# Performance work log

Hardware: AMD Instinct MI355X
Metric: run time of the kernel (lower is better)

The kernel has to match this reference:

```python
import jax, jax.numpy as jnp
import numpy as np

B, T, C = 8, 1024, 768
H, D = 12, 64

def setup_inputs() -> dict:
    key = jax.random.key(0)
    ks = jax.random.split(key, 6)
    s = 0.02
    return {
        "x": jax.random.normal(ks[0], (B, T, C), dtype=jnp.float32),
        "Wq": jax.random.normal(ks[1], (H, C, D), dtype=jnp.float32) * s,
        "Wk": jax.random.normal(ks[2], (H, C, D), dtype=jnp.float32) * s,
        "Wv": jax.random.normal(ks[3], (H, C, D), dtype=jnp.float32) * s,
        "Wproj": jax.random.normal(ks[4], (C, C), dtype=jnp.float32) * s,
        "bproj": jnp.zeros((C,), dtype=jnp.float32),
    }

def reference(x, Wq, Wk, Wv, Wproj, bproj):
    # per-head projections, vectorized over heads: [B,H,T,D]
    q = jnp.einsum('btc,hcd->bhtd', x, Wq)
    k = jnp.einsum('btc,hcd->bhtd', x, Wk)
    v = jnp.einsum('btc,hcd->bhtd', x, Wv)
    scale = 1.0 / jnp.sqrt(jnp.asarray(q.shape[-1], q.dtype))
    scores = jnp.einsum('bhtd,bhsd->bhts', q, k) * scale  # [B,H,T,T]
    attn = jax.nn.softmax(scores, axis=-1)
    out = jnp.einsum('bhts,bhsd->bhtd', attn, v)          # [B,H,T,D]
    # concat heads along last dim -> [B,T,H*D]
    out = out.transpose(0, 2, 1, 3).reshape(x.shape[0], x.shape[1], -1)
    return out @ Wproj + bproj
```

## Files before the change

### kernel.cpp

```cpp
#include <hip/hip_runtime.h>
#include <hip/hip_bf16.h>

using u16 = unsigned short;

typedef __attribute__((ext_vector_type(8))) short bf16x8;
typedef __attribute__((ext_vector_type(4))) float f32x4;
typedef __attribute__((ext_vector_type(16))) float f32x16;

#define B_ 8
#define T_ 1024
#define C_ 768
#define H_ 12
#define D_ 64

typedef const void __attribute__((address_space(1))) gv_t;
typedef void __attribute__((address_space(3))) lv_t;

__device__ __forceinline__ void gload_lds16(const void* g, void* l) {
  __builtin_amdgcn_global_load_lds((gv_t*)g, (lv_t*)l, 16, 0, 0);
}

__device__ __forceinline__ u16 f2b(float f) {
  union { float f; unsigned u; } a; a.f = f;
  unsigned r = a.u + 0x7FFFu + ((a.u >> 16) & 1u);
  return (u16)(r >> 16);
}

__device__ __forceinline__ float fexp2(float x) {
  float r;
  asm("v_exp_f32 %0, %1" : "=v"(r) : "v"(x));
  return r;
}

__device__ __forceinline__ unsigned cvtpk_bf16(float lo, float hi) {
  unsigned r;
  asm("v_cvt_pk_bf16_f32 %0, %1, %2" : "=v"(r) : "v"(lo), "v"(hi));
  return r;
}
__device__ __forceinline__ void plane32_swap(unsigned &a, unsigned &b) {
  asm volatile("v_permlane32_swap_b32 %0, %1" : "+v"(a), "+v"(b));
}

__global__ __launch_bounds__(256) void prep_all(
    const float* __restrict__ x,
    const float* __restrict__ Wq, const float* __restrict__ Wk,
    const float* __restrict__ Wv, const float* __restrict__ Wp,
    u16* __restrict__ Xb, u16* __restrict__ Wqkvt, u16* __restrict__ Wpt)
{
  int bb = blockIdx.x;
  if (bb < 3072) {
    int i = (bb * 256 + threadIdx.x) * 8;
    float4 a = *(const float4*)(x + i);
    float4 b = *(const float4*)(x + i + 4);
    union { bf16x8 v; u16 s[8]; } o;
    o.s[0] = f2b(a.x); o.s[1] = f2b(a.y); o.s[2] = f2b(a.z); o.s[3] = f2b(a.w);
    o.s[4] = f2b(b.x); o.s[5] = f2b(b.y); o.s[6] = f2b(b.z); o.s[7] = f2b(b.w);
    *(bf16x8*)(Xb + i) = o.v;
  } else {
    int idx = (bb - 3072) * 256 + threadIdx.x;
    int p = idx / 147456;
    int r = idx - p * 147456;
    if (p < 3) {
      const float* W = (p == 0) ? Wq : ((p == 1) ? Wk : Wv);
      int d4 = r & 15;
      int c  = (r >> 4) % 768;
      int h  = r / 12288;
      float4 v = *(const float4*)(W + (size_t)h * 49152 + (size_t)c * 64 + d4 * 4);
      size_t nb = (size_t)p * 589824 + ((size_t)h * 64 + d4 * 4) * 768 + c;
      Wqkvt[nb]           = f2b(v.x);
      Wqkvt[nb + 768]     = f2b(v.y);
      Wqkvt[nb + 1536]    = f2b(v.z);
      Wqkvt[nb + 2304]    = f2b(v.w);
    } else {
      int co4 = r % 192;
      int ci  = r / 192;
      float4 v = *(const float4*)(Wp + (size_t)ci * 768 + co4 * 4);
      size_t ob = (size_t)(co4 * 4) * 768 + ci;
      Wpt[ob]        = f2b(v.x);
      Wpt[ob + 768]  = f2b(v.y);
      Wpt[ob + 1536] = f2b(v.z);
      Wpt[ob + 2304] = f2b(v.w);
    }
  }
}

#define GEMM_MAINLOOP(APTR, BPTR, KDIM)                                          \
  {                                                                              \
    _Pragma("unroll")                                                            \
    for (int q = 0; q < 2; ++q) {                                                \
      int db = q * 4096 + t * 16;                                                \
      int row = db >> 6;                                                         \
      int cb = (db ^ ((row & 3) << 4)) & 63;                                     \
      gload_lds16((const char*)(APTR) + ((size_t)(m0 + row) * (KDIM)) * 2 + cb,  \
                  (char*)As + db);                                               \
      gload_lds16((const char*)(BPTR) + ((size_t)(n0 + row) * (KDIM)) * 2 + cb,  \
                  (char*)Bs + db);                                               \
    }                                                                            \
    const int NIT = (KDIM) / 32;                                                 \
    for (int it = 0; it < NIT; ++it) {                                           \
      const int cur = it & 1;                                                    \
      asm volatile("s_waitcnt vmcnt(0)" ::: "memory");                           \
      __syncthreads();                                                           \
      if (it + 1 < NIT) {                                                        \
        int k0 = (it + 1) * 32;                                                  \
        int nb = (cur ^ 1) * 8192;                                               \
        _Pragma("unroll")                                                        \
        for (int q = 0; q < 2; ++q) {                                            \
          int db = q * 4096 + t * 16;                                            \
          int row = db >> 6;                                                     \
          int cb = (db ^ ((row & 3) << 4)) & 63;                                 \
          gload_lds16((const char*)(APTR) + ((size_t)(m0 + row) * (KDIM) + k0) * 2 + cb, \
                      (char*)As + nb + db);                                      \
          gload_lds16((const char*)(BPTR) + ((size_t)(n0 + row) * (KDIM) + k0) * 2 + cb, \
                      (char*)Bs + nb + db);                                      \
        }                                                                        \
      }                                                                          \
      const char* Ab = (const char*)As + cur * 8192;                             \
      const char* Bb = (const char*)Bs + cur * 8192;                             \
      bf16x8 af[4], bfr[4];                                                      \
      _Pragma("unroll")                                                          \
      for (int i = 0; i < 4; ++i) {                                              \
        int ra = wr + i * 16 + lr;                                               \
        int Ua = ra * 64 + hc;                                                   \
        af[i] = *(const bf16x8*)(Ab + (Ua ^ ((ra & 3) << 4)));                   \
        int rb = wc + i * 16 + lr;                                               \
        int Ub = rb * 64 + hc;                                                   \
        bfr[i] = *(const bf16x8*)(Bb + (Ub ^ ((rb & 3) << 4)));                  \
      }                                                                          \
      _Pragma("unroll")                                                          \
      for (int i = 0; i < 4; ++i)                                                \
        _Pragma("unroll")                                                        \
        for (int j = 0; j < 4; ++j)                                              \
          acc[i][j] = __builtin_amdgcn_mfma_f32_16x16x32_bf16(af[i], bfr[j],     \
                                                              acc[i][j], 0, 0, 0); \
    }                                                                            \
  }

__global__ __launch_bounds__(256) void gemm_qkv(
    const u16* __restrict__ X, const u16* __restrict__ Wt,
    u16* __restrict__ Qw, u16* __restrict__ Kw, u16* __restrict__ Vt)
{
  __shared__ __align__(16) u16 As[2 * 128 * 32];
  __shared__ __align__(16) u16 Bs[2 * 128 * 32];
  const int t = threadIdx.x;
  const int l = t & 63, w = t >> 6;
  const int lr = l & 15;
  const int hc = (l >> 4) * 16;
  const int m0 = blockIdx.x * 128;
  const int n0 = blockIdx.y * 128;
  const int wr = (w >> 1) * 64, wc = (w & 1) * 64;

  f32x4 acc[4][4] = {};
  GEMM_MAINLOOP(X, Wt, 768)

  #pragma unroll
  for (int j = 0; j < 4; ++j) {
    int col_g = n0 + wc + j * 16 + lr;
    int p = (col_g >= 1536) ? 2 : ((col_g >= 768) ? 1 : 0);
    int rr = col_g - p * 768;
    int h = rr >> 6, d = rr & 63;
    #pragma unroll
    for (int i = 0; i < 4; ++i) {
      int rg0 = m0 + wr + i * 16 + ((l >> 4) << 2);
      int b = rg0 >> 10, tt = rg0 & 1023;
      if (p == 0) {
        size_t base = (((size_t)b * H_ + h) * T_ + tt) * D_ + d;
        #pragma unroll
        for (int r = 0; r < 4; ++r)
          Qw[base + (size_t)r * D_] = f2b(acc[i][j][r] * 0.18033688f);
      } else if (p == 1) {
        size_t base = (((size_t)b * H_ + h) * T_ + tt) * D_ + d;
        #pragma unroll
        for (int r = 0; r < 4; ++r) Kw[base + (size_t)r * D_] = f2b(acc[i][j][r]);
      } else {
        unsigned long long pk =
            (unsigned long long)f2b(acc[i][j][0]) |
            ((unsigned long long)f2b(acc[i][j][1]) << 16) |
            ((unsigned long long)f2b(acc[i][j][2]) << 32) |
            ((unsigned long long)f2b(acc[i][j][3]) << 48);
        *reinterpret_cast<unsigned long long*>(
            &Vt[(((size_t)b * H_ + h) * D_ + d) * T_ + tt]) = pk;
      }
    }
  }
}

__global__ __launch_bounds__(256) void gemm_proj(
    const u16* __restrict__ A, const u16* __restrict__ Wt,
    const float* __restrict__ bias, float* __restrict__ O)
{
  __shared__ __align__(16) u16 As[2 * 128 * 32];
  __shared__ __align__(16) u16 Bs[2 * 128 * 32];
  const int t = threadIdx.x;
  const int l = t & 63, w = t >> 6;
  const int lr = l & 15;
  const int hc = (l >> 4) * 16;
  const int m0 = blockIdx.x * 128;
  const int n0 = blockIdx.y * 128;
  const int wr = (w >> 1) * 64, wc = (w & 1) * 64;

  f32x4 acc[4][4] = {};
  GEMM_MAINLOOP(A, Wt, 768)

  #pragma unroll
  for (int j = 0; j < 4; ++j) {
    int col_g = n0 + wc + j * 16 + lr;
    float bb = bias[col_g];
    #pragma unroll
    for (int i = 0; i < 4; ++i) {
      int rg0 = m0 + wr + i * 16 + ((l >> 4) << 2);
      #pragma unroll
      for (int r = 0; r < 4; ++r)
        O[(size_t)(rg0 + r) * C_ + col_g] = acc[i][j][r] + bb;
    }
  }
}

__global__ __launch_bounds__(256) void attn_fwd(
    const u16* __restrict__ Qw, const u16* __restrict__ Kw,
    const u16* __restrict__ VT, u16* __restrict__ AO)
{
  __shared__ __align__(16) u16 Ks[2][64 * 64];
  __shared__ __align__(16) u16 Vs[3][64 * 64];
  const int t = threadIdx.x, l = t & 63;
  const int lq = l & 31, lh = l >> 5;

  const int bid = blockIdx.x;
  const int bh = (bid & 7) * 12 + ((bid >> 3) >> 3);
  const int qt = (bid >> 3) & 7;
  const int b = bh / H_, h = bh - b * H_;
  const u16* Qh = Qw + (size_t)bh * (T_ * D_);
  const char* Kp = (const char*)(Kw + (size_t)bh * (T_ * D_));
  const char* Vp = (const char*)(VT + (size_t)bh * (D_ * T_));
  const int q0w = qt * 128 + (t >> 6) * 32;
  const int qrow = q0w + lq;

  bf16x8 qf[4];
  #pragma unroll
  for (int ks = 0; ks < 4; ++ks)
    qf[ks] = *(const bf16x8*)(Qh + (size_t)qrow * D_ + lh * 8 + ks * 16);

  bf16x8 ones;
  {
    union { u16 s[8]; bf16x8 v; } u;
    #pragma unroll
    for (int j = 0; j < 8; ++j) u.s[j] = 0x3F80;
    ones = u.v;
  }

  f32x16 oA = {}, oB = {}, lacc = {};
  bf16x8 pbP[4];

  const int db0 = t * 16, db1 = 4096 + t * 16;
  const int row0 = db0 >> 7, row1 = db1 >> 7;
  const int cb0 = (db0 ^ ((row0 & 7) << 4)) & 127;
  const int cb1 = (db1 ^ ((row1 & 7) << 4)) & 127;

#define ISSUE_TILE(KT, KB, VB)                                                   \
  gload_lds16(Kp + (size_t)((KT) + row0) * 128 + cb0, (char*)Ks[KB] + db0);      \
  gload_lds16(Kp + (size_t)((KT) + row1) * 128 + cb1, (char*)Ks[KB] + db1);      \
  gload_lds16(Vp + (size_t)row0 * 2048 + (KT) * 2 + cb0, (char*)Vs[VB] + db0);   \
  gload_lds16(Vp + (size_t)row1 * 2048 + (KT) * 2 + cb1, (char*)Vs[VB] + db1);

  ISSUE_TILE(0, 0, 0)

  int wv = 1, pv = 2;

  for (int kt_i = 0; kt_i < 16; ++kt_i) {
    const int cur = kt_i & 1;
    asm volatile("s_waitcnt vmcnt(0)" ::: "memory");
    __syncthreads();
    if (kt_i < 15) { ISSUE_TILE((kt_i + 1) * 64, cur ^ 1, wv) }

    f32x16 sA = {}, sB = {};
    {
      bf16x8 ka[4];
      #pragma unroll
      for (int ks = 0; ks < 4; ++ks) {
        int row = lq;
        int U = row * 128 + ks * 32 + lh * 16;
        ka[ks] = *(const bf16x8*)((const char*)Ks[cur] + (U ^ ((row & 7) << 4)));
      }
      #pragma unroll
      for (int ks = 0; ks < 4; ++ks)
        sA = __builtin_amdgcn_mfma_f32_32x32x16_bf16(ka[ks], qf[ks], sA, 0, 0, 0);
      #pragma unroll
      for (int ks = 0; ks < 4; ++ks) {
        int row = lq + 32;
        int U = row * 128 + ks * 32 + lh * 16;
        ka[ks] = *(const bf16x8*)((const char*)Ks[cur] + (U ^ ((row & 7) << 4)));
      }
      #pragma unroll
      for (int ks = 0; ks < 4; ++ks)
        sB = __builtin_amdgcn_mfma_f32_32x32x16_bf16(ka[ks], qf[ks], sB, 0, 0, 0);
    }

    if (kt_i > 0) {
      const char* Vb = (const char*)Vs[pv];
      bf16x8 va[4];
      #pragma unroll
      for (int ks = 0; ks < 4; ++ks) {
        int row = lq;
        int U = row * 128 + ks * 32 + lh * 16;
        va[ks] = *(const bf16x8*)(Vb + (U ^ ((row & 7) << 4)));
      }
      #pragma unroll
      for (int ks = 0; ks < 4; ++ks)
        oA = __builtin_amdgcn_mfma_f32_32x32x16_bf16(va[ks], pbP[ks], oA, 0, 0, 0);
      #pragma unroll
      for (int ks = 0; ks < 4; ++ks) {
        int row = lq + 32;
        int U = row * 128 + ks * 32 + lh * 16;
        va[ks] = *(const bf16x8*)(Vb + (U ^ ((row & 7) << 4)));
      }
      #pragma unroll
      for (int ks = 0; ks < 4; ++ks)
        oB = __builtin_amdgcn_mfma_f32_32x32x16_bf16(va[ks], pbP[ks], oB, 0, 0, 0);
      #pragma unroll
      for (int ks = 0; ks < 4; ++ks)
        lacc = __builtin_amdgcn_mfma_f32_32x32x16_bf16(ones, pbP[ks], lacc, 0, 0, 0);
    }

    #pragma unroll
    for (int r = 0; r < 16; ++r) {
      sA[r] = fexp2(sA[r]);
      sB[r] = fexp2(sB[r]);
    }

    #pragma unroll
    for (int ks = 0; ks < 4; ++ks) {
      f32x16& S = (ks < 2) ? sA : sB;
      const int g = (ks & 1) * 8;
      unsigned a0 = cvtpk_bf16(S[g + 0], S[g + 1]);
      unsigned a1 = cvtpk_bf16(S[g + 2], S[g + 3]);
      unsigned b0 = cvtpk_bf16(S[g + 4], S[g + 5]);
      unsigned b1 = cvtpk_bf16(S[g + 6], S[g + 7]);
      plane32_swap(a0, b0);
      plane32_swap(a1, b1);
      union { unsigned wd[4]; bf16x8 v; } u;
      u.wd[0] = a0; u.wd[1] = a1; u.wd[2] = b0; u.wd[3] = b1;
      pbP[ks] = u.v;
    }

    wv = (wv == 2) ? 0 : wv + 1;
    pv = (pv == 2) ? 0 : pv + 1;
  }
#undef ISSUE_TILE

  {
    const char* Vb = (const char*)Vs[pv];
    bf16x8 va[4];
    #pragma unroll
    for (int ks = 0; ks < 4; ++ks) {
      int row = lq;
      int U = row * 128 + ks * 32 + lh * 16;
      va[ks] = *(const bf16x8*)(Vb + (U ^ ((row & 7) << 4)));
    }
    #pragma unroll
    for (int ks = 0; ks < 4; ++ks)
      oA = __builtin_amdgcn_mfma_f32_32x32x16_bf16(va[ks], pbP[ks], oA, 0, 0, 0);
    #pragma unroll
    for (int ks = 0; ks < 4; ++ks) {
      int row = lq + 32;
      int U = row * 128 + ks * 32 + lh * 16;
      va[ks] = *(const bf16x8*)(Vb + (U ^ ((row & 7) << 4)));
    }
    #pragma unroll
    for (int ks = 0; ks < 4; ++ks)
      oB = __builtin_amdgcn_mfma_f32_32x32x16_bf16(va[ks], pbP[ks], oB, 0, 0, 0);
    #pragma unroll
    for (int ks = 0; ks < 4; ++ks)
      lacc = __builtin_amdgcn_mfma_f32_32x32x16_bf16(ones, pbP[ks], lacc, 0, 0, 0);
  }

  float inv = 1.0f / lacc[0];
  size_t base = ((size_t)b * T_ + qrow) * C_ + h * D_;
  #pragma unroll
  for (int dh = 0; dh < 2; ++dh) {
    const f32x16& OO = dh ? oB : oA;
    #pragma unroll
    for (int g = 0; g < 4; ++g) {
      int d0 = 8 * g + 4 * lh + 32 * dh;
      unsigned long long pk =
          (unsigned long long)f2b(OO[4 * g + 0] * inv) |
          ((unsigned long long)f2b(OO[4 * g + 1] * inv) << 16) |
          ((unsigned long long)f2b(OO[4 * g + 2] * inv) << 32) |
          ((unsigned long long)f2b(OO[4 * g + 3] * inv) << 48);
      *reinterpret_cast<unsigned long long*>(&AO[base + d0]) = pk;
    }
  }
}

extern "C" void kernel_launch(void* const* d_in, const int* in_sizes, int n_in,
                              void* d_out, int out_size, void* d_ws, size_t ws_size,
                              hipStream_t stream) {
  (void)in_sizes; (void)n_in; (void)out_size;
  const float* x     = (const float*)d_in[0];
  const float* Wq    = (const float*)d_in[1];
  const float* Wk    = (const float*)d_in[2];
  const float* Wv    = (const float*)d_in[3];
  const float* Wproj = (const float*)d_in[4];
  const float* bproj = (const float*)d_in[5];

  const size_t NEEDED = 55050240;
  if (ws_size < NEEDED) return;

  char* ws = (char*)d_ws;
  u16* Wpt   = (u16*)(ws);
  u16* Qw    = (u16*)(ws + 1179648);
  u16* Kw    = (u16*)(ws + 13762560);
  u16* Vt    = (u16*)(ws + 26345472);
  u16* Xb    = (u16*)(ws + 38928384);
  u16* AO    = (u16*)(ws + 38928384);
  u16* Wqkvt = (u16*)(ws + 51511296);

  prep_all<<<dim3(5376), dim3(256), 0, stream>>>(x, Wq, Wk, Wv, Wproj, Xb, Wqkvt, Wpt);
  gemm_qkv<<<dim3(64, 18), dim3(256), 0, stream>>>(Xb, Wqkvt, Qw, Kw, Vt);
  attn_fwd<<<dim3(768), dim3(256), 0, stream>>>(Qw, Kw, Vt, AO);
  gemm_proj<<<dim3(64, 6), dim3(256), 0, stream>>>(AO, Wpt, bproj, (float*)d_out);
}
```

Baseline: 133.4 us.

## Replace double-buffered GEMM loop with single-buffered BK=64 tiles and larger QKV block

Removes the shared double-buffered GEMM macro. Both GEMMs now use a single-buffered loop with K-step 64 and an 8-way XOR swizzle, which halves the number of barrier iterations but no longer overlaps global loads with MFMA work. The QKV GEMM also grows to 512 threads with a 256x128 tile, so each weight tile loaded into LDS is reused across twice as many rows. The risk is exposed load latency, since each iteration waits for its own loads before computing.

Result: faster. 127.9 us (-4.1%).

```diff
diff --git a/kernel.cpp b/kernel.cpp
--- a/kernel.cpp
+++ b/kernel.cpp
@@ -84,74 +84,63 @@
   }
 }
 
-#define GEMM_MAINLOOP(APTR, BPTR, KDIM)                                          \
-  {                                                                              \
-    _Pragma("unroll")                                                            \
-    for (int q = 0; q < 2; ++q) {                                                \
-      int db = q * 4096 + t * 16;                                                \
-      int row = db >> 6;                                                         \
-      int cb = (db ^ ((row & 3) << 4)) & 63;                                     \
-      gload_lds16((const char*)(APTR) + ((size_t)(m0 + row) * (KDIM)) * 2 + cb,  \
-                  (char*)As + db);                                               \
-      gload_lds16((const char*)(BPTR) + ((size_t)(n0 + row) * (KDIM)) * 2 + cb,  \
-                  (char*)Bs + db);                                               \
-    }                                                                            \
-    const int NIT = (KDIM) / 32;                                                 \
-    for (int it = 0; it < NIT; ++it) {                                           \
-      const int cur = it & 1;                                                    \
-      asm volatile("s_waitcnt vmcnt(0)" ::: "memory");                           \
-      __syncthreads();                                                           \
-      if (it + 1 < NIT) {                                                        \
-        int k0 = (it + 1) * 32;                                                  \
-        int nb = (cur ^ 1) * 8192;                                               \
-        _Pragma("unroll")                                                        \
-        for (int q = 0; q < 2; ++q) {                                            \
-          int db = q * 4096 + t * 16;                                            \
-          int row = db >> 6;                                                     \
-          int cb = (db ^ ((row & 3) << 4)) & 63;                                 \
-          gload_lds16((const char*)(APTR) + ((size_t)(m0 + row) * (KDIM) + k0) * 2 + cb, \
-                      (char*)As + nb + db);                                      \
-          gload_lds16((const char*)(BPTR) + ((size_t)(n0 + row) * (KDIM) + k0) * 2 + cb, \
-                      (char*)Bs + nb + db);                                      \
-        }                                                                        \
-      }                                                                          \
-      const char* Ab = (const char*)As + cur * 8192;                             \
-      const char* Bb = (const char*)Bs + cur * 8192;                             \
-      bf16x8 af[4], bfr[4];                                                      \
-      _Pragma("unroll")                                                          \
-      for (int i = 0; i < 4; ++i) {                                              \
-        int ra = wr + i * 16 + lr;                                               \
-        int Ua = ra * 64 + hc;                                                   \
-        af[i] = *(const bf16x8*)(Ab + (Ua ^ ((ra & 3) << 4)));                   \
-        int rb = wc + i * 16 + lr;                                               \
-        int Ub = rb * 64 + hc;                                                   \
-        bfr[i] = *(const bf16x8*)(Bb + (Ub ^ ((rb & 3) << 4)));                  \
-      }                                                                          \
-      _Pragma("unroll")                                                          \
-      for (int i = 0; i < 4; ++i)                                                \
-        _Pragma("unroll")                                                        \
-        for (int j = 0; j < 4; ++j)                                              \
-          acc[i][j] = __builtin_amdgcn_mfma_f32_16x16x32_bf16(af[i], bfr[j],     \
-                                                              acc[i][j], 0, 0, 0); \
-    }                                                                            \
-  }
-
-__global__ __launch_bounds__(256) void gemm_qkv(
+__global__ __launch_bounds__(512) void gemm_qkv(
     const u16* __restrict__ X, const u16* __restrict__ Wt,
     u16* __restrict__ Qw, u16* __restrict__ Kw, u16* __restrict__ Vt)
 {
-  __shared__ __align__(16) u16 As[2 * 128 * 32];
-  __shared__ __align__(16) u16 Bs[2 * 128 * 32];
+  __shared__ __align__(16) u16 As[256 * 64];
+  __shared__ __align__(16) u16 Bs[128 * 64];
   const int t = threadIdx.x;
   const int l = t & 63, w = t >> 6;
   const int lr = l & 15;
   const int hc = (l >> 4) * 16;
-  const int m0 = blockIdx.x * 128;
+  const int m0 = blockIdx.x * 256;
   const int n0 = blockIdx.y * 128;
-  const int wr = (w >> 1) * 64, wc = (w & 1) * 64;
+  const int wr = (w >> 1) * 64;
+  const int wc = (w & 1) * 64;
 
   f32x4 acc[4][4] = {};
-  GEMM_MAINLOOP(X, Wt, 768)
+
+  for (int k0 = 0; k0 < 768; k0 += 64) {
+    #pragma unroll
+    for (int q = 0; q < 4; ++q) {
+      int db = q * 8192 + t * 16;
+      int row = db >> 7;
+      int cb = (db ^ ((row & 7) << 4)) & 127;
+      gload_lds16((const char*)X + ((size_t)(m0 + row) * 768 + k0) * 2 + cb,
+                  (char*)As + db);
+    }
+    #pragma unroll
+    for (int q = 0; q < 2; ++q) {
+      int db = q * 8192 + t * 16;
+      int row = db >> 7;
+      int cb = (db ^ ((row & 7) << 4)) & 127;
+      gload_lds16((const char*)Wt + ((size_t)(n0 + row) * 768 + k0) * 2 + cb,
+                  (char*)Bs + db);
+    }
+    asm volatile("s_waitcnt vmcnt(0)" ::: "memory");
+    __syncthreads();
+    #pragma unroll
+    for (int kq = 0; kq < 2; ++kq) {
+      bf16x8 af[4], bfr[4];
+      #pragma unroll
+      for (int i = 0; i < 4; ++i) {
+        int ra = wr + i * 16 + lr;
+        int Ua = ra * 128 + kq * 64 + hc;
+        af[i] = *(const bf16x8*)((const char*)As + (Ua ^ ((ra & 7) << 4)));
+        int rb = wc + i * 16 + lr;
+        int Ub = rb * 128 + kq * 64 + hc;
+        bfr[i] = *(const bf16x8*)((const char*)Bs + (Ub ^ ((rb & 7) << 4)));
+      }
+      #pragma unroll
+      for (int i = 0; i < 4; ++i)
+        #pragma unroll
+        for (int j = 0; j < 4; ++j)
+          acc[i][j] = __builtin_amdgcn_mfma_f32_16x16x32_bf16(af[i], bfr[j],
+                                                              acc[i][j], 0, 0, 0);
+    }
+    __syncthreads();
+  }
 
   #pragma unroll
   for (int j = 0; j < 4; ++j) {
@@ -189,8 +178,8 @@
     const u16* __restrict__ A, const u16* __restrict__ Wt,
     const float* __restrict__ bias, float* __restrict__ O)
 {
-  __shared__ __align__(16) u16 As[2 * 128 * 32];
-  __shared__ __align__(16) u16 Bs[2 * 128 * 32];
+  __shared__ __align__(16) u16 As[128 * 64];
+  __shared__ __align__(16) u16 Bs[128 * 64];
   const int t = threadIdx.x;
   const int l = t & 63, w = t >> 6;
   const int lr = l & 15;
@@ -200,7 +189,40 @@
   const int wr = (w >> 1) * 64, wc = (w & 1) * 64;
 
   f32x4 acc[4][4] = {};
-  GEMM_MAINLOOP(A, Wt, 768)
+  for (int k0 = 0; k0 < 768; k0 += 64) {
+    #pragma unroll
+    for (int q = 0; q < 4; ++q) {
+      int db = q * 4096 + t * 16;
+      int row = db >> 7;
+      int cb = (db ^ ((row & 7) << 4)) & 127;
+      gload_lds16((const char*)A + ((size_t)(m0 + row) * 768 + k0) * 2 + cb,
+                  (char*)As + db);
+      gload_lds16((const char*)Wt + ((size_t)(n0 + row) * 768 + k0) * 2 + cb,
+                  (char*)Bs + db);
+    }
+    asm volatile("s_waitcnt vmcnt(0)" ::: "memory");
+    __syncthreads();
+    #pragma unroll
+    for (int kq = 0; kq < 2; ++kq) {
+      bf16x8 af[4], bfr[4];
+      #pragma unroll
+      for (int i = 0; i < 4; ++i) {
+        int ra = wr + i * 16 + lr;
+        int Ua = ra * 128 + kq * 64 + hc;
+        af[i] = *(const bf16x8*)((const char*)As + (Ua ^ ((ra & 7) << 4)));
+        int rb = wc + i * 16 + lr;
+        int Ub = rb * 128 + kq * 64 + hc;
+        bfr[i] = *(const bf16x8*)((const char*)Bs + (Ub ^ ((rb & 7) << 4)));
+      }
+      #pragma unroll
+      for (int i = 0; i < 4; ++i)
+        #pragma unroll
+        for (int j = 0; j < 4; ++j)
+          acc[i][j] = __builtin_amdgcn_mfma_f32_16x16x32_bf16(af[i], bfr[j],
+                                                              acc[i][j], 0, 0, 0);
+    }
+    __syncthreads();
+  }
 
   #pragma unroll
   for (int j = 0; j < 4; ++j) {
@@ -415,7 +437,7 @@
   u16* Wqkvt = (u16*)(ws + 51511296);
 
   prep_all<<<dim3(5376), dim3(256), 0, stream>>>(x, Wq, Wk, Wv, Wproj, Xb, Wqkvt, Wpt);
-  gemm_qkv<<<dim3(64, 18), dim3(256), 0, stream>>>(Xb, Wqkvt, Qw, Kw, Vt);
+  gemm_qkv<<<dim3(32, 18), dim3(512), 0, stream>>>(Xb, Wqkvt, Qw, Kw, Vt);
   attn_fwd<<<dim3(768), dim3(256), 0, stream>>>(Qw, Kw, Vt, AO);
   gemm_proj<<<dim3(64, 6), dim3(256), 0, stream>>>(AO, Wpt, bproj, (float*)d_out);
 }
```
